# Kernel optimization log

Measured on AMD Instinct MI355X. Metric: run time of the kernel, lower is better.

## Reference

```python
import jax, jax.numpy as jnp
import numpy as np

B, L, HID = 4, 4096, 1024
H, D = 16, 64  # num_heads, head_dim


def setup_inputs() -> dict:
    key = jax.random.key(0)
    ks = jax.random.split(key, 5)
    s = 1.0 / np.sqrt(HID)
    mk = lambda k: jax.random.uniform(k, (HID, HID), minval=-s, maxval=s, dtype=jnp.float32)
    return {
        "x": jax.random.normal(ks[0], (B, L, HID), dtype=jnp.float32),
        "Wq": mk(ks[1]), "bq": jnp.zeros((HID,), jnp.float32),
        "Wk": mk(ks[2]), "bk": jnp.zeros((HID,), jnp.float32),
        "Wv": mk(ks[3]), "bv": jnp.zeros((HID,), jnp.float32),
        "Wo": mk(ks[4]), "bo": jnp.zeros((HID,), jnp.float32),
    }


def reference(x, Wq, bq, Wk, bk, Wv, bv, Wo, bo):
    Bx, Lx, _ = x.shape
    # projections (weights stored [in, out])
    q = (x @ Wq + bq).reshape(Bx, Lx, H, D)
    k = (x @ Wk + bk).reshape(Bx, Lx, H, D)
    v = (x @ Wv + bv).reshape(Bx, Lx, H, D)
    # Single window (L <= window_size): torch matmul batches over (B, L) and
    # contracts head_dim -> per-token head-to-head scores [B, L, H, H].
    scores = jnp.einsum('blhd,bled->blhe', q, k) / np.sqrt(D).astype(np.float32)
    probs = jax.nn.softmax(scores, axis=-1)
    out = jnp.einsum('blhe,bled->blhd', probs, v).reshape(Bx, Lx, HID)
    return out @ Wo + bo
```

## Files before the change

kernel.cpp:

```cpp
#include <hip/hip_runtime.h>
#include <stdint.h>


typedef __attribute__((ext_vector_type(8))) short short8;
typedef __attribute__((ext_vector_type(4))) float floatx4;
typedef __attribute__((address_space(1))) unsigned int gu32;
typedef __attribute__((address_space(3))) unsigned int lu32;

#define HID 1024
#define MTOK 16384
#define WELEM (HID * HID)
#define XELEM (MTOK * HID)

#define SBAR() __builtin_amdgcn_s_barrier()
#define WAITLGKM() do { asm volatile("s_waitcnt lgkmcnt(0)" ::: "memory"); \
                        __builtin_amdgcn_sched_barrier(0); } while (0)
#define VMCNT(n) do { asm volatile("s_waitcnt vmcnt(" #n ")" ::: "memory"); \
                      __builtin_amdgcn_sched_barrier(0); } while (0)

__device__ __forceinline__ unsigned short f2bf(float f) {
  union { float f; uint32_t u; } v; v.f = f;
  uint32_t u = v.u;
  u += 0x7fffu + ((u >> 16) & 1u);
  return (unsigned short)(u >> 16);
}

__global__ __launch_bounds__(256) void cvt_x_kernel(const float* __restrict__ x,
                                                    unsigned short* __restrict__ xb) {
  const int idx = blockIdx.x * 256 + threadIdx.x;
  float4 v = ((const float4*)x)[idx];
  ushort4 o;
  o.x = f2bf(v.x); o.y = f2bf(v.y); o.z = f2bf(v.z); o.w = f2bf(v.w);
  ((ushort4*)xb)[idx] = o;
}

__global__ __launch_bounds__(256) void cvt_w_kernel(const float* __restrict__ W0,
                                                    const float* __restrict__ W1,
                                                    const float* __restrict__ W2,
                                                    const float* __restrict__ W3,
                                                    unsigned short* __restrict__ WT) {
  const float* W = (blockIdx.z == 0) ? W0 : (blockIdx.z == 1) ? W1
                   : (blockIdx.z == 2) ? W2 : W3;
  unsigned short* out = WT + (size_t)blockIdx.z * WELEM;
  __shared__ float tile[64][65];
  const int t = threadIdx.x;
  const int n0 = blockIdx.x * 64, k0 = blockIdx.y * 64;
#pragma unroll
  for (int i = 0; i < 4; i++) {
    const int row = i * 16 + (t >> 4);
    const int col = (t & 15) * 4;
    float4 v = *(const float4*)&W[(size_t)(k0 + row) * HID + n0 + col];
    tile[row][col] = v.x; tile[row][col + 1] = v.y;
    tile[row][col + 2] = v.z; tile[row][col + 3] = v.w;
  }
  __syncthreads();
#pragma unroll
  for (int i = 0; i < 4; i++) {
    const int n = i * 16 + (t >> 4);
    const int k = (t & 15) * 4;
    ushort4 o;
    o.x = f2bf(tile[k][n]);     o.y = f2bf(tile[k + 1][n]);
    o.z = f2bf(tile[k + 2][n]); o.w = f2bf(tile[k + 3][n]);
    *(ushort4*)&out[(size_t)(n0 + n) * HID + k0 + k] = o;
  }
}

template <bool QKV>
__global__ __launch_bounds__(512, 2) void gemm256(
    const unsigned short* __restrict__ A,
    const unsigned short* __restrict__ BTb,
    const float* __restrict__ b0, const float* __restrict__ b1,
    const float* __restrict__ b2,
    void* __restrict__ Cv)
{
  __shared__ short8 smem_[131072 / 16];
  char* smem = (char*)smem_;

  constexpr int R = QKV ? 3 : 1;
  const int bid = blockIdx.x;
  const int xcd = bid & 7;
  const int j = bid >> 3;
  const int nb0 = j >> 3;
  const int mb = xcd * 8 + (j & 7);
  const int m0 = mb * 256;
  const int cb = nb0 * 256;

  const unsigned short* BT0 = QKV ? BTb : (BTb + (size_t)3 * WELEM);

  const int t_ = threadIdx.x;
  const int wv = t_ >> 6, lane = t_ & 63;
  const int quad = lane >> 4, r16 = lane & 15;
  const int wm = wv >> 2, wn = wv & 3;

  const int srow = wv * 16 + (lane >> 2);
  const int scol = ((lane & 3) ^ ((lane >> 3) & 3)) * 8;
  const unsigned short* Ag = A + (size_t)(m0 + srow) * HID + scol;
  const unsigned short* Bg = BT0 + (size_t)(cb + srow) * HID + scol;

  const int qsw = (quad ^ ((r16 >> 1) & 3)) << 4;
  const char* Ard = smem + wm * 16384 + r16 * 64 + qsw;
  const char* Brd = smem + 32768 + (wn >> 1) * 16384 + ((wn & 1) * 64 + r16) * 64 + qsw;

  floatx4 acc[8][4] = {};

  auto stageA = [&](int h, int tt) {
    const unsigned short* s = Ag + (size_t)h * 128 * HID + tt * 64;
    char* d = smem + ((tt & 1) << 16) + h * 16384 + wv * 1024;
    __builtin_amdgcn_global_load_lds((const gu32*)s,        (lu32*)d,          16, 0, 0);
    __builtin_amdgcn_global_load_lds((const gu32*)(s + 32), (lu32*)(d + 8192), 16, 0, 0);
  };
  auto stageB = [&](int h, int tt) {
    const unsigned short* s = Bg + (size_t)h * 128 * HID + tt * 64;
    char* d = smem + ((tt & 1) << 16) + 32768 + h * 16384 + wv * 1024;
    __builtin_amdgcn_global_load_lds((const gu32*)s,        (lu32*)d,          16, 0, 0);
    __builtin_amdgcn_global_load_lds((const gu32*)(s + 32), (lu32*)(d + 8192), 16, 0, 0);
  };

  const int NT = HID / 64;

  short8 a[4][2];
  short8 b23[2][2];
  short8 bA[2][2], bB[2][2];

  auto TILE = [&](int t, int bufb, int othb, short8 (&bc)[2][2], short8 (&bn)[2][2]) {
    if (t + 1 < NT) stageA(0, t + 1);
#pragma unroll
    for (int ks = 0; ks < 2; ++ks)
#pragma unroll
      for (int mi = 0; mi < 4; ++mi)
        a[mi][ks] = *(const short8*)(Ard + bufb + ks * 8192 + mi * 1024);
    SBAR();
    __builtin_amdgcn_s_setprio(1);
#pragma unroll
    for (int ks = 0; ks < 2; ++ks)
#pragma unroll
      for (int mi = 0; mi < 4; ++mi)
#pragma unroll
        for (int ni = 0; ni < 2; ++ni)
          acc[mi][ni] = __builtin_amdgcn_mfma_f32_16x16x32_bf16(a[mi][ks], bc[ni][ks], acc[mi][ni], 0, 0, 0);
    __builtin_amdgcn_s_setprio(0);
    WAITLGKM();

    if (t + 1 < NT) stageA(1, t + 1);
#pragma unroll
    for (int ks = 0; ks < 2; ++ks)
#pragma unroll
      for (int ni = 0; ni < 2; ++ni)
        b23[ni][ks] = *(const short8*)(Brd + bufb + ks * 8192 + (2 + ni) * 1024);
    SBAR();
    __builtin_amdgcn_s_setprio(1);
#pragma unroll
    for (int ks = 0; ks < 2; ++ks)
#pragma unroll
      for (int mi = 0; mi < 4; ++mi)
#pragma unroll
        for (int ni = 0; ni < 2; ++ni)
          acc[mi][2 + ni] = __builtin_amdgcn_mfma_f32_16x16x32_bf16(a[mi][ks], b23[ni][ks], acc[mi][2 + ni], 0, 0, 0);
    __builtin_amdgcn_s_setprio(0);
    WAITLGKM();

    if (t + 2 < NT) stageB(0, t + 2);
#pragma unroll
    for (int ks = 0; ks < 2; ++ks)
#pragma unroll
      for (int mi = 0; mi < 4; ++mi)
        a[mi][ks] = *(const short8*)(Ard + bufb + ks * 8192 + (4 + mi) * 1024);
    if (t + 2 < NT)      { VMCNT(6); }
    else if (t + 1 < NT) { VMCNT(4); }
    SBAR();
    __builtin_amdgcn_s_setprio(1);
#pragma unroll
    for (int ks = 0; ks < 2; ++ks)
#pragma unroll
      for (int mi = 0; mi < 4; ++mi)
#pragma unroll
        for (int ni = 0; ni < 2; ++ni)
          acc[4 + mi][2 + ni] = __builtin_amdgcn_mfma_f32_16x16x32_bf16(a[mi][ks], b23[ni][ks], acc[4 + mi][2 + ni], 0, 0, 0);
    __builtin_amdgcn_s_setprio(0);
    WAITLGKM();

    if (t + 2 < NT) stageB(1, t + 2);
    if (t + 1 < NT) {
#pragma unroll
      for (int ks = 0; ks < 2; ++ks)
#pragma unroll
        for (int ni = 0; ni < 2; ++ni)
          bn[ni][ks] = *(const short8*)(Brd + othb + ks * 8192 + ni * 1024);
    }
    if (t + 2 < NT)      { VMCNT(4); }
    else if (t + 1 < NT) { VMCNT(0); }
    SBAR();
    __builtin_amdgcn_s_setprio(1);
#pragma unroll
    for (int ks = 0; ks < 2; ++ks)
#pragma unroll
      for (int mi = 0; mi < 4; ++mi)
#pragma unroll
        for (int ni = 0; ni < 2; ++ni)
          acc[4 + mi][ni] = __builtin_amdgcn_mfma_f32_16x16x32_bf16(a[mi][ks], bc[ni][ks], acc[4 + mi][ni], 0, 0, 0);
    __builtin_amdgcn_s_setprio(0);
    WAITLGKM();
  };

  stageA(0, 0); stageA(1, 0); stageB(0, 0); stageB(1, 0);
  stageB(0, 1); stageB(1, 1);
  VMCNT(4);
  SBAR();
#pragma unroll
  for (int ks = 0; ks < 2; ++ks)
#pragma unroll
    for (int ni = 0; ni < 2; ++ni)
      bA[ni][ks] = *(const short8*)(Brd + ks * 8192 + ni * 1024);

  for (int r = 0; r < R; ++r) {
    for (int t = 0; t < NT; t += 2) {
      TILE(t,     0,       0x10000, bA, bB);
      TILE(t + 1, 0x10000, 0,       bB, bA);
    }

    if (r + 1 < R) {
      Bg += WELEM;
      stageA(0, 0); stageA(1, 0); stageB(0, 0); stageB(1, 0);
      stageB(0, 1); stageB(1, 1);
    }

    {
      const float* bias = QKV ? ((r == 0) ? b0 : ((r == 1) ? b1 : b2)) : b0;
      float bvv[4];
#pragma unroll
      for (int ni = 0; ni < 4; ++ni) bvv[ni] = bias[cb + wn * 64 + ni * 16 + r16];

      const int row0 = m0 + wm * 128 + quad * 4;
      unsigned short* outb = (unsigned short*)Cv + (size_t)r * XELEM;
      float* outf = (float*)Cv;
#pragma unroll
      for (int mi = 0; mi < 8; ++mi) {
#pragma unroll
        for (int rr = 0; rr < 4; ++rr) {
          const size_t roff = (size_t)(row0 + mi * 16 + rr) * HID + cb + wn * 64 + r16;
#pragma unroll
          for (int ni = 0; ni < 4; ++ni) {
            const float val = acc[mi][ni][rr] + bvv[ni];
            if constexpr (QKV) outb[roff + ni * 16] = f2bf(val);
            else               outf[roff + ni * 16] = val;
          }
        }
      }
    }

    if (r + 1 < R) {
#pragma unroll
      for (int mi = 0; mi < 8; ++mi)
#pragma unroll
        for (int ni = 0; ni < 4; ++ni)
          acc[mi][ni] = floatx4{0.f, 0.f, 0.f, 0.f};
      VMCNT(0);
      SBAR();
#pragma unroll
      for (int ks = 0; ks < 2; ++ks)
#pragma unroll
        for (int ni = 0; ni < 2; ++ni)
          bA[ni][ks] = *(const short8*)(Brd + ks * 8192 + ni * 1024);
    }
  }
}

__global__ __launch_bounds__(256) void attn_kernel(const unsigned short* qkv,
                                                   unsigned short* attn) {
  __shared__ unsigned short vls[4][1056];
  __shared__ unsigned short pls[4][16 * 24];

  const int t = threadIdx.x;
  const int wv = t >> 6, lane = t & 63;
  const int quad = lane >> 4, r16 = lane & 15;
  const size_t base = ((size_t)blockIdx.x * 4 + wv) * HID;
  const unsigned short* qp = qkv + base;
  const unsigned short* kp = qkv + (size_t)XELEM + base;
  const unsigned short* vp = qkv + 2 * (size_t)XELEM + base;

  __builtin_amdgcn_global_load_lds((const gu32*)(vp + lane * 8),       (lu32*)&vls[wv][0],   16, 0, 0);
  __builtin_amdgcn_global_load_lds((const gu32*)(vp + 512 + lane * 8), (lu32*)&vls[wv][528], 16, 0, 0);

  short8 qf0 = *(const short8*)(qp + r16 * 64 + quad * 8);
  short8 qf1 = *(const short8*)(qp + r16 * 64 + quad * 8 + 32);
  short8 kf0 = *(const short8*)(kp + r16 * 64 + quad * 8);
  short8 kf1 = *(const short8*)(kp + r16 * 64 + quad * 8 + 32);

  floatx4 sc = {0.f, 0.f, 0.f, 0.f};
  sc = __builtin_amdgcn_mfma_f32_16x16x32_bf16(qf0, kf0, sc, 0, 0, 0);
  sc = __builtin_amdgcn_mfma_f32_16x16x32_bf16(qf1, kf1, sc, 0, 0, 0);

#pragma unroll
  for (int rr = 0; rr < 4; rr++) {
    float s = sc[rr] * 0.125f;
    float m = s;
#pragma unroll
    for (int off = 1; off < 16; off <<= 1) m = fmaxf(m, __shfl_xor(m, off));
    float ex = __expf(s - m);
    float sum = ex;
#pragma unroll
    for (int off = 1; off < 16; off <<= 1) sum += __shfl_xor(sum, off);
    pls[wv][(quad * 4 + rr) * 24 + r16] = f2bf(ex / sum);
  }

  __syncthreads();

  const short8 zero8 = {0, 0, 0, 0, 0, 0, 0, 0};
  short8 af = zero8;
  short8 bf[4] = {zero8, zero8, zero8, zero8};
  if (quad < 2) {
    af = *(const short8*)&pls[wv][r16 * 24 + quad * 8];
#pragma unroll
    for (int c = 0; c < 4; c++)
#pragma unroll
      for (int jj = 0; jj < 8; jj++)
        bf[c][jj] = (short)vls[wv][quad * 528 + jj * 64 + c * 16 + r16];
  }

  floatx4 ov[4];
#pragma unroll
  for (int c = 0; c < 4; c++) {
    floatx4 z = {0.f, 0.f, 0.f, 0.f};
    ov[c] = __builtin_amdgcn_mfma_f32_16x16x32_bf16(af, bf[c], z, 0, 0, 0);
  }

#pragma unroll
  for (int rr = 0; rr < 4; rr++)
#pragma unroll
    for (int c = 0; c < 4; c++)
      attn[base + (size_t)(quad * 4 + rr) * 64 + c * 16 + r16] = f2bf(ov[c][rr]);
}

extern "C" void kernel_launch(void* const* d_in, const int* in_sizes, int n_in,
                              void* d_out, int out_size, void* d_ws, size_t ws_size,
                              hipStream_t stream) {
  const float* x  = (const float*)d_in[0];
  const float* Wq = (const float*)d_in[1];
  const float* bq = (const float*)d_in[2];
  const float* Wk = (const float*)d_in[3];
  const float* bk = (const float*)d_in[4];
  const float* Wv = (const float*)d_in[5];
  const float* bv = (const float*)d_in[6];
  const float* Wo = (const float*)d_in[7];
  const float* bo = (const float*)d_in[8];

  char* ws = (char*)d_ws;
  unsigned short* xb  = (unsigned short*)ws;
  unsigned short* wt  = (unsigned short*)(ws + (size_t)XELEM * 2);
  unsigned short* qkv = wt + 4 * (size_t)WELEM;

  cvt_x_kernel<<<XELEM / 1024, 256, 0, stream>>>(x, xb);
  cvt_w_kernel<<<dim3(16, 16, 4), 256, 0, stream>>>(Wq, Wk, Wv, Wo, wt);
  gemm256<true><<<256, 512, 0, stream>>>(xb, wt, bq, bk, bv, (void*)qkv);
  attn_kernel<<<4096, 256, 0, stream>>>(qkv, qkv);
  gemm256<false><<<256, 512, 0, stream>>>(qkv, wt, bo, bo, bo, d_out);
}
```

Baseline: 292.0 us.

## Restructure GEMM main loop to single-tile prefetch depth with A-fragment register reuse

```diff
diff --git a/kernel.cpp b/kernel.cpp
--- a/kernel.cpp
+++ b/kernel.cpp
@@ -118,110 +118,109 @@
 
   const int NT = HID / 64;
 
-  short8 a[4][2];
-  short8 b23[2][2];
-  short8 bA[2][2], bB[2][2];
-
-  auto TILE = [&](int t, int bufb, int othb, short8 (&bc)[2][2], short8 (&bn)[2][2]) {
-    if (t + 1 < NT) stageA(0, t + 1);
-#pragma unroll
-    for (int ks = 0; ks < 2; ++ks)
-#pragma unroll
-      for (int mi = 0; mi < 4; ++mi)
-        a[mi][ks] = *(const short8*)(Ard + bufb + ks * 8192 + mi * 1024);
-    SBAR();
-    __builtin_amdgcn_s_setprio(1);
-#pragma unroll
-    for (int ks = 0; ks < 2; ++ks)
-#pragma unroll
-      for (int mi = 0; mi < 4; ++mi)
+  short8 alo[4][2], ahi[4][2];
+  short8 b01[2][2], b23[2][2];
+
+  stageA(0, 0); stageA(1, 0); stageB(0, 0); stageB(1, 0);
+  VMCNT(0);
+  SBAR();
+#pragma unroll
+  for (int ks = 0; ks < 2; ++ks)
+#pragma unroll
+    for (int mi = 0; mi < 4; ++mi)
+      alo[mi][ks] = *(const short8*)(Ard + ks * 8192 + mi * 1024);
+
+  for (int r = 0; r < R; ++r) {
+    for (int t = 0; t < NT; ++t) {
+      const int bufb = (t & 1) << 16;
+      const int nxtb = bufb ^ 0x10000;
+      const bool more = (t + 1 < NT);
+
+      if (more) { stageA(0, t + 1); VMCNT(2); } else { VMCNT(0); }
+      SBAR();
+#pragma unroll
+      for (int ks = 0; ks < 2; ++ks)
 #pragma unroll
         for (int ni = 0; ni < 2; ++ni)
-          acc[mi][ni] = __builtin_amdgcn_mfma_f32_16x16x32_bf16(a[mi][ks], bc[ni][ks], acc[mi][ni], 0, 0, 0);
-    __builtin_amdgcn_s_setprio(0);
-    WAITLGKM();
-
-    if (t + 1 < NT) stageA(1, t + 1);
-#pragma unroll
-    for (int ks = 0; ks < 2; ++ks)
-#pragma unroll
-      for (int ni = 0; ni < 2; ++ni)
-        b23[ni][ks] = *(const short8*)(Brd + bufb + ks * 8192 + (2 + ni) * 1024);
-    SBAR();
-    __builtin_amdgcn_s_setprio(1);
-#pragma unroll
-    for (int ks = 0; ks < 2; ++ks)
-#pragma unroll
-      for (int mi = 0; mi < 4; ++mi)
+          b01[ni][ks] = *(const short8*)(Brd + bufb + ks * 8192 + ni * 1024);
+#pragma unroll
+      for (int ks = 0; ks < 2; ++ks)
 #pragma unroll
         for (int ni = 0; ni < 2; ++ni)
-          acc[mi][2 + ni] = __builtin_amdgcn_mfma_f32_16x16x32_bf16(a[mi][ks], b23[ni][ks], acc[mi][2 + ni], 0, 0, 0);
-    __builtin_amdgcn_s_setprio(0);
-    WAITLGKM();
-
-    if (t + 2 < NT) stageB(0, t + 2);
-#pragma unroll
-    for (int ks = 0; ks < 2; ++ks)
-#pragma unroll
-      for (int mi = 0; mi < 4; ++mi)
-        a[mi][ks] = *(const short8*)(Ard + bufb + ks * 8192 + (4 + mi) * 1024);
-    if (t + 2 < NT)      { VMCNT(6); }
-    else if (t + 1 < NT) { VMCNT(4); }
-    SBAR();
-    __builtin_amdgcn_s_setprio(1);
-#pragma unroll
-    for (int ks = 0; ks < 2; ++ks)
-#pragma unroll
-      for (int mi = 0; mi < 4; ++mi)
-#pragma unroll
-        for (int ni = 0; ni < 2; ++ni)
-          acc[4 + mi][2 + ni] = __builtin_amdgcn_mfma_f32_16x16x32_bf16(a[mi][ks], b23[ni][ks], acc[4 + mi][2 + ni], 0, 0, 0);
-    __builtin_amdgcn_s_setprio(0);
-    WAITLGKM();
-
-    if (t + 2 < NT) stageB(1, t + 2);
-    if (t + 1 < NT) {
-#pragma unroll
-      for (int ks = 0; ks < 2; ++ks)
-#pragma unroll
-        for (int ni = 0; ni < 2; ++ni)
-          bn[ni][ks] = *(const short8*)(Brd + othb + ks * 8192 + ni * 1024);
-    }
-    if (t + 2 < NT)      { VMCNT(4); }
-    else if (t + 1 < NT) { VMCNT(0); }
-    SBAR();
-    __builtin_amdgcn_s_setprio(1);
-#pragma unroll
-    for (int ks = 0; ks < 2; ++ks)
-#pragma unroll
-      for (int mi = 0; mi < 4; ++mi)
-#pragma unroll
-        for (int ni = 0; ni < 2; ++ni)
-          acc[4 + mi][ni] = __builtin_amdgcn_mfma_f32_16x16x32_bf16(a[mi][ks], bc[ni][ks], acc[4 + mi][ni], 0, 0, 0);
-    __builtin_amdgcn_s_setprio(0);
-    WAITLGKM();
-  };
-
-  stageA(0, 0); stageA(1, 0); stageB(0, 0); stageB(1, 0);
-  stageB(0, 1); stageB(1, 1);
-  VMCNT(4);
-  SBAR();
-#pragma unroll
-  for (int ks = 0; ks < 2; ++ks)
-#pragma unroll
-    for (int ni = 0; ni < 2; ++ni)
-      bA[ni][ks] = *(const short8*)(Brd + ks * 8192 + ni * 1024);
-
-  for (int r = 0; r < R; ++r) {
-    for (int t = 0; t < NT; t += 2) {
-      TILE(t,     0,       0x10000, bA, bB);
-      TILE(t + 1, 0x10000, 0,       bB, bA);
+          b23[ni][ks] = *(const short8*)(Brd + bufb + ks * 8192 + (2 + ni) * 1024);
+      __builtin_amdgcn_s_setprio(1);
+#pragma unroll
+      for (int ks = 0; ks < 2; ++ks)
+#pragma unroll
+        for (int mi = 0; mi < 4; ++mi)
+#pragma unroll
+          for (int ni = 0; ni < 2; ++ni)
+            acc[mi][ni] = __builtin_amdgcn_mfma_f32_16x16x32_bf16(alo[mi][ks], b01[ni][ks], acc[mi][ni], 0, 0, 0);
+      __builtin_amdgcn_s_setprio(0);
+      WAITLGKM();
+
+      if (more) stageA(1, t + 1);
+      SBAR();
+#pragma unroll
+      for (int ks = 0; ks < 2; ++ks)
+#pragma unroll
+        for (int mi = 0; mi < 4; ++mi)
+          ahi[mi][ks] = *(const short8*)(Ard + bufb + ks * 8192 + (4 + mi) * 1024);
+      __builtin_amdgcn_s_setprio(1);
+#pragma unroll
+      for (int ks = 0; ks < 2; ++ks)
+#pragma unroll
+        for (int mi = 0; mi < 4; ++mi)
+#pragma unroll
+          for (int ni = 0; ni < 2; ++ni)
+            acc[mi][2 + ni] = __builtin_amdgcn_mfma_f32_16x16x32_bf16(alo[mi][ks], b23[ni][ks], acc[mi][2 + ni], 0, 0, 0);
+      __builtin_amdgcn_s_setprio(0);
+      WAITLGKM();
+
+      if (more) { stageB(0, t + 1); VMCNT(4); }
+      SBAR();
+      if (more) {
+#pragma unroll
+        for (int ks = 0; ks < 2; ++ks)
+#pragma unroll
+          for (int mi = 0; mi < 2; ++mi)
+            alo[mi][ks] = *(const short8*)(Ard + nxtb + ks * 8192 + mi * 1024);
+      }
+      __builtin_amdgcn_s_setprio(1);
+#pragma unroll
+      for (int ks = 0; ks < 2; ++ks)
+#pragma unroll
+        for (int mi = 0; mi < 4; ++mi)
+#pragma unroll
+          for (int ni = 0; ni < 2; ++ni)
+            acc[4 + mi][2 + ni] = __builtin_amdgcn_mfma_f32_16x16x32_bf16(ahi[mi][ks], b23[ni][ks], acc[4 + mi][2 + ni], 0, 0, 0);
+      __builtin_amdgcn_s_setprio(0);
+      WAITLGKM();
+
+      if (more) stageB(1, t + 1);
+      SBAR();
+      if (more) {
+#pragma unroll
+        for (int ks = 0; ks < 2; ++ks)
+#pragma unroll
+          for (int mi = 2; mi < 4; ++mi)
+            alo[mi][ks] = *(const short8*)(Ard + nxtb + ks * 8192 + mi * 1024);
+      }
+      __builtin_amdgcn_s_setprio(1);
+#pragma unroll
+      for (int ks = 0; ks < 2; ++ks)
+#pragma unroll
+        for (int mi = 0; mi < 4; ++mi)
+#pragma unroll
+          for (int ni = 0; ni < 2; ++ni)
+            acc[4 + mi][ni] = __builtin_amdgcn_mfma_f32_16x16x32_bf16(ahi[mi][ks], b01[ni][ks], acc[4 + mi][ni], 0, 0, 0);
+      __builtin_amdgcn_s_setprio(0);
+      WAITLGKM();
     }
 
     if (r + 1 < R) {
       Bg += WELEM;
       stageA(0, 0); stageA(1, 0); stageB(0, 0); stageB(1, 0);
-      stageB(0, 1); stageB(1, 1);
     }
 
     {
@@ -259,8 +258,8 @@
 #pragma unroll
       for (int ks = 0; ks < 2; ++ks)
 #pragma unroll
-        for (int ni = 0; ni < 2; ++ni)
-          bA[ni][ks] = *(const short8*)(Brd + ks * 8192 + ni * 1024);
+        for (int mi = 0; mi < 4; ++mi)
+          alo[mi][ks] = *(const short8*)(Ard + ks * 8192 + mi * 1024);
     }
   }
 }
```

Result: no change. 287.2 us (-1.6%).
